# Optimization experiments

Hardware: AMD Instinct MI355X
Metric: run time of the kernel (lower is better)

## Reference

```python
import jax, jax.numpy as jnp
import numpy as np

VOCAB, EMB, HID, DSEM, TK, B, MAX_OOV = 50000, 128, 512, 256, 400, 64, 100


def _linear(x, W, b=None):
    y = x @ W.T
    return y if b is None else y + b


def setup_inputs() -> dict:
    key = jax.random.key(0)
    ks = jax.random.split(key, 32)
    s = 0.02
    inp = {
        "y_t_1": jax.random.randint(ks[0], (B,), 0, VOCAB),
        "s_h": jax.random.normal(ks[1], (1, B, HID)) * 0.1,
        "s_c": jax.random.normal(ks[2], (1, B, HID)) * 0.1,
        "encoder_outputs": jax.random.normal(ks[3], (B, TK, 2 * HID)) * 0.1,
        "encoder_feature": jax.random.normal(ks[4], (B * TK, 2 * HID)) * 0.1,
        "enc_padding_mask": jnp.ones((B, TK), jnp.float32),
        "c_t_1": jax.random.normal(ks[5], (B, 2 * HID)) * 0.1,
        "extra_zeros": jnp.zeros((B, MAX_OOV), jnp.float32),
        "enc_batch_extend_vocab": jax.random.randint(ks[6], (B, TK), 0, VOCAB + MAX_OOV),
        "coverage": jax.random.uniform(ks[7], (B, TK)),
        "step": 1,
        "ri": jax.random.normal(ks[8], (B, TK, 2 * DSEM)) * 0.1,
        # parameters (torch Linear convention: weight is (out, in))
        "emb_W": jax.random.normal(ks[9], (VOCAB, EMB)) * s,
        "Ws_W": jax.random.normal(ks[10], (2 * HID, 2 * HID)) * s,
        "Ws_b": jax.random.normal(ks[11], (2 * HID,)) * s,
        "v_W": jax.random.normal(ks[12], (1, 2 * HID)) * s,
        "Wc_W": jax.random.normal(ks[13], (2 * HID, 1)) * s,
        "Wr_W": jax.random.normal(ks[14], (2 * HID, 2 * DSEM)) * s,
        "xc_W": jax.random.normal(ks[15], (EMB, 2 * HID + EMB)) * s,
        "xc_b": jax.random.normal(ks[16], (EMB,)) * s,
        "W_ih": jax.random.uniform(ks[17], (4 * HID, EMB), minval=-0.02, maxval=0.02),
        "W_hh": jax.random.uniform(ks[18], (4 * HID, HID), minval=-0.02, maxval=0.02),
        "b_ih": jnp.concatenate([jnp.zeros(HID), jnp.ones(HID), jnp.zeros(2 * HID)]),
        "b_hh": jnp.zeros((4 * HID,), jnp.float32),
        "pg_W": jax.random.normal(ks[19], (1, 4 * HID + EMB)) * s,
        "pg_b": jax.random.normal(ks[20], (1,)) * s,
        "o1_W": jax.random.normal(ks[21], (HID, 3 * HID)) * s,
        "o1_b": jax.random.normal(ks[22], (HID,)) * s,
        "o2_W": jax.random.normal(ks[23], (VOCAB, HID)) * s,
        "o2_b": jax.random.normal(ks[24], (VOCAB,)) * s,
    }
    return inp


def _attention(s_t_hat, encoder_outputs, encoder_feature, enc_padding_mask, coverage, ri,
               Ws_W, Ws_b, v_W, Wc_W, Wr_W):
    b, t_k, n = encoder_outputs.shape
    dec_fea = _linear(s_t_hat, Ws_W, Ws_b)                     # (b, 2h)
    att = encoder_feature.reshape(b, t_k, n) + dec_fea[:, None, :]
    att = att + coverage[..., None] * Wc_W[:, 0]                # coverage feature
    scores = jnp.tanh(att) @ v_W[0]                             # (b, t_k)
    attn = jax.nn.softmax(scores, axis=1) * enc_padding_mask
    attn = attn / attn.sum(1, keepdims=True)
    c_t = jnp.einsum('bt,btn->bn', attn, encoder_outputs)
    coverage_next = coverage + attn
    # structural attention (not renormalized in the original)
    att2 = jnp.einsum('btd,nd->btn', ri, Wr_W) + dec_fea[:, None, :]
    scores2 = jnp.tanh(att2) @ v_W[0]
    a_struct = jax.nn.softmax(scores2, axis=1) * enc_padding_mask
    c_struct = jnp.einsum('bt,btn->bn', a_struct, encoder_outputs)
    return c_t, attn, coverage_next, c_struct, a_struct


def reference(y_t_1, s_h, s_c, encoder_outputs, encoder_feature, enc_padding_mask,
              c_t_1, extra_zeros, enc_batch_extend_vocab, coverage, step, ri,
              emb_W, Ws_W, Ws_b, v_W, Wc_W, Wr_W, xc_W, xc_b,
              W_ih, W_hh, b_ih, b_hh, pg_W, pg_b, o1_W, o1_b, o2_W, o2_b):
    b = y_t_1.shape[0]
    # embed + context projection
    y_emb = emb_W[y_t_1]                                        # (b, emb)
    x = _linear(jnp.concatenate([c_t_1, y_emb], 1), xc_W, xc_b)  # (b, emb)
    # single-step LSTM (torch gate order i,f,g,o)
    h0, c0 = s_h[0], s_c[0]
    gates = x @ W_ih.T + b_ih + h0 @ W_hh.T + b_hh
    i, f, g, o = jnp.split(gates, 4, axis=1)
    c_new = jax.nn.sigmoid(f) * c0 + jax.nn.sigmoid(i) * jnp.tanh(g)
    h_new = jax.nn.sigmoid(o) * jnp.tanh(c_new)
    s_t_hat = jnp.concatenate([h_new, c_new], 1)                # (b, 2h)
    c_t, attn_dist, coverage_next, c_struct, _ = _attention(
        s_t_hat, encoder_outputs, encoder_feature, enc_padding_mask, coverage, ri,
        Ws_W, Ws_b, v_W, Wc_W, Wr_W)
    coverage_out = coverage_next  # training / step>0 path
    # pointer-generator gate
    p_gen = jax.nn.sigmoid(_linear(jnp.concatenate([c_struct, s_t_hat, x], 1), pg_W, pg_b))
    out = _linear(jnp.concatenate([h_new, c_struct], 1), o1_W, o1_b)
    out = _linear(out, o2_W, o2_b)
    vocab_dist = jax.nn.softmax(out, axis=1)
    vocab_dist_ = p_gen * vocab_dist
    attn_ = (1.0 - p_gen) * attn_dist
    ext = jnp.concatenate([vocab_dist_, extra_zeros], 1)        # (b, vocab+oov)
    rows = jnp.arange(b)[:, None]
    final_dist = ext.at[rows, enc_batch_extend_vocab].add(attn_)
    return (final_dist, h_new[None], c_new[None], c_t, attn_dist, p_gen, coverage_out)
```

## Files before the change

### kernel.cpp

```cpp
#include <hip/hip_runtime.h>
#include <hip/hip_bf16.h>
#include <math.h>

#define BATCH  64
#define EMB    128
#define HID    512
#define TK     400
#define VOCAB  50000
#define MAX_OOV 100
#define VEXT   50100
#define H2     1024
#define K_RI   512

typedef short  bf16x8 __attribute__((ext_vector_type(8)));
typedef float  f32x4  __attribute__((ext_vector_type(4)));
typedef unsigned short u16x8 __attribute__((ext_vector_type(8)));

__device__ __forceinline__ unsigned short f2b(float f){
  unsigned u = __float_as_uint(f);
  u += 0x7fffu + ((u >> 16) & 1u);
  return (unsigned short)(u >> 16);
}
__device__ __forceinline__ float sigm(float x){ return 1.0f/(1.0f+expf(-x)); }
__device__ __forceinline__ float clampf(float x, float lo, float hi){ return fminf(fmaxf(x, lo), hi); }
__device__ __forceinline__ float fast_tanh(float x){
  float e = __expf(2.f*x);
  return 1.f - 2.f/(e + 1.f);
}
__device__ __forceinline__ bf16x8 ld_frag(const unsigned short* p){
  return __builtin_bit_cast(bf16x8, *(const u16x8*)p);
}
__device__ __forceinline__ u16x8 cvt8(const float4 a, const float4 b){
  u16x8 r;
  r[0]=f2b(a.x); r[1]=f2b(a.y); r[2]=f2b(a.z); r[3]=f2b(a.w);
  r[4]=f2b(b.x); r[5]=f2b(b.y); r[6]=f2b(b.z); r[7]=f2b(b.w);
  return r;
}

#define WS_X        0
#define WS_H        8192
#define WS_STHAT    73728
#define WS_DECFEA   139264
#define WS_SCORES   204800
#define WS_SCORES2  230400
#define WS_ATTN     256000
#define WS_ASTRUCT  281600
#define WS_CSTRUCT  307200
#define WS_PGEN     372736
#define WS_OUT1BF   372800
#define WS_ROWMAX   389184
#define WS_ROWSUM   389248
#define WS_PMAX     WS_SCORES
#define WS_PSUM     (WS_SCORES+512)

#define OUT_FINAL 0
#define OUT_H     3206400
#define OUT_C     3239168
#define OUT_CT    3271936
#define OUT_ATTN  3337472
#define OUT_PGEN  3363072
#define OUT_COV   3363136
#define OUT_WR16  131072
#define CTX_CT    0
#define CTX_CS    262144

__global__ __launch_bounds__(256) void k_wrcvt(const float* __restrict__ Wr,
    unsigned short* __restrict__ WrF){
  int t = blockIdx.x*256 + threadIdx.x;
  int lane = t & 63;
  int f    = (t >> 6) & 15;
  int nb   = t >> 10;
  int r  = nb*16 + (lane & 15);
  int k0 = f*32 + (lane >> 4)*8;
  const float4* p = (const float4*)(Wr + (size_t)r*512 + k0);
  *(u16x8*)(WrF + (size_t)t*8) = cvt8(p[0], p[1]);
}

__global__ __launch_bounds__(256) void k_embx(
    const int* __restrict__ y, const float* __restrict__ embW,
    const float* __restrict__ ct1, const float* __restrict__ xcW,
    const float* __restrict__ xcb, float* __restrict__ ws)
{
  __shared__ float vec[1152];
  int b = blockIdx.x, q = blockIdx.y, tid = threadIdx.x;
  int yb = y[b];
  for (int i = tid; i < 1024; i += 256) vec[i] = ct1[b*1024+i];
  if (tid < 128) vec[1024+tid] = embW[(size_t)yb*128+tid];
  __syncthreads();
  int wave = tid>>6, lane = tid&63;
  #pragma unroll 2
  for (int oo = 0; oo < 8; ++oo){
    int o = q*32 + wave*8 + oo;
    const float* row = xcW + (size_t)o*1152;
    float acc = 0.f;
    #pragma unroll
    for (int i=0;i<18;i++) acc += row[lane + 64*i] * vec[lane + 64*i];
    for (int off=32; off>0; off>>=1) acc += __shfl_down(acc, off);
    if (lane==0) ws[WS_X + b*128 + o] = xcb[o] + acc;
  }
}

__global__ __launch_bounds__(256) void k_gates(
    const float* __restrict__ Wih, const float* __restrict__ Whh,
    const float* __restrict__ bih, const float* __restrict__ bhh,
    const float* __restrict__ sh, const float* __restrict__ ws,
    float* __restrict__ gates)
{
  __shared__ float xh[640];
  int b = blockIdx.x, gc = blockIdx.y, tid = threadIdx.x;
  for (int i=tid;i<128;i+=256) xh[i] = ws[WS_X + b*128 + i];
  for (int i=tid;i<512;i+=256) xh[128+i] = sh[b*512+i];
  __syncthreads();
  int wave = tid>>6, lane = tid&63;
  int gbase = gc*128 + wave*32;
  for (int gg=0; gg<32; ++gg){
    int g = gbase + gg;
    const float* ri = Wih + (size_t)g*128;
    const float* rh = Whh + (size_t)g*512;
    float acc = ri[lane]*xh[lane] + ri[lane+64]*xh[lane+64];
    #pragma unroll
    for (int i=0;i<8;i++) acc += rh[lane + 64*i] * xh[128 + lane + 64*i];
    for (int off=32; off>0; off>>=1) acc += __shfl_down(acc, off);
    if (lane==0) gates[b*2048 + g] = acc + bih[g] + bhh[g];
  }
}

__global__ __launch_bounds__(256) void k_lstmpt(
    const float* __restrict__ gates, const float* __restrict__ sc,
    float* __restrict__ ws, float* __restrict__ outh, float* __restrict__ outc)
{
  int b = blockIdx.x, tid = threadIdx.x;
  const float* g = gates + b*2048;
  for (int j = tid; j < 512; j += 256){
    float ig = sigm(g[j]),       fg = sigm(g[512+j]);
    float gg = tanhf(g[1024+j]), og = sigm(g[1536+j]);
    float c0 = sc[b*512+j];
    float cn = fg*c0 + ig*gg;
    float hn = og*tanhf(cn);
    ws[WS_H + b*512+j] = hn;
    ws[WS_STHAT + b*1024 + j] = hn; ws[WS_STHAT + b*1024 + 512 + j] = cn;
    outh[b*512+j] = hn; outc[b*512+j] = cn;
  }
}

__global__ __launch_bounds__(256) void k_decfea(const float* __restrict__ WsW,
    const float* __restrict__ Wsb, float* __restrict__ ws){
  __shared__ float st[1024];
  int b = blockIdx.x, q = blockIdx.y, tid = threadIdx.x;
  for (int i=tid;i<1024;i+=256) st[i] = ws[WS_STHAT + b*1024 + i];
  __syncthreads();
  int wave = tid>>6, lane = tid&63;
  for (int oo=0; oo<64; ++oo){
    int n = q*256 + wave*64 + oo;
    const float* row = WsW + (size_t)n*1024;
    float acc = 0.f;
    #pragma unroll
    for (int i=0;i<16;i++) acc += row[lane + 64*i] * st[lane + 64*i];
    for (int off=32; off>0; off>>=1) acc += __shfl_down(acc, off);
    if (lane==0) ws[WS_DECFEA + b*1024 + n] = Wsb[n] + acc;
  }
}

__global__ __launch_bounds__(256) void k_scores1(const float* __restrict__ ef,
    const float* __restrict__ cov, const float* __restrict__ vW,
    const float* __restrict__ WcW, float* __restrict__ ws){
  __shared__ float df[1024], vv[1024], wc[1024];
  int b = blockIdx.x, tid = threadIdx.x;
  for (int i=tid;i<1024;i+=256){ df[i]=ws[WS_DECFEA+b*1024+i]; vv[i]=vW[i]; wc[i]=WcW[i]; }
  __syncthreads();
  int wave = tid>>6, lane = tid&63;
  int t = blockIdx.y*4 + wave;
  float cv = cov[b*400+t];
  const float4* e = (const float4*)(ef + (size_t)(b*400+t)*1024 + lane*16);
  float4 e0 = e[0], e1 = e[1], e2 = e[2], e3 = e[3];
  float ebuf[16] = {e0.x,e0.y,e0.z,e0.w, e1.x,e1.y,e1.z,e1.w,
                    e2.x,e2.y,e2.z,e2.w, e3.x,e3.y,e3.z,e3.w};
  float acc = 0.f;
  int base = lane*16;
  #pragma unroll
  for (int j=0;j<16;j++){ int n=base+j; acc += fast_tanh(ebuf[j] + df[n] + cv*wc[n]) * vv[n]; }
  for (int off=32; off>0; off>>=1) acc += __shfl_down(acc, off, 64);
  if (lane==0) ws[WS_SCORES + b*400 + t] = clampf(acc, -64.f, 64.f);
}

__global__ __launch_bounds__(256) void k_scores2(const float* __restrict__ ri,
    const unsigned short* __restrict__ WrF, const float* __restrict__ vW,
    float* __restrict__ ws){
  __shared__ __align__(16) unsigned short Bs[2][16384];
  int tid = threadIdx.x, lane = tid & 63, w = tid >> 6;
  int m0 = blockIdx.x*64 + w*16;
  int fr = lane & 15, fq8 = (lane >> 4)*8;
  int cq = lane >> 4, cr = lane & 15;

  bf16x8 a[16];
  {
    const float* p = ri + (size_t)(m0 + fr)*K_RI + fq8;
    #pragma unroll
    for (int f=0; f<16; f++){
      float4 x0 = *(const float4*)(p + f*32);
      float4 x1 = *(const float4*)(p + f*32 + 4);
      a[f] = __builtin_bit_cast(bf16x8, cvt8(x0, x1));
    }
  }

  const float* decfea = ws + WS_DECFEA;
  int dfo[4];
  #pragma unroll
  for (int rg=0; rg<4; rg++) dfo[rg] = ((m0 + cq*4 + rg)/400)*1024;
  float sa[4] = {0.f,0.f,0.f,0.f};

  #pragma unroll
  for (int i=0;i<8;i++){
    int e = (i*256 + tid)*8;
    __builtin_amdgcn_global_load_lds(
      (const __attribute__((address_space(1))) unsigned int*)(WrF + e),
      (__attribute__((address_space(3))) unsigned int*)&Bs[0][e], 16, 0, 0);
  }

  for (int p=0; p<32; ++p){
    __syncthreads();
    if (p < 31){
      const unsigned short* src = WrF + (size_t)(p+1)*16384;
      unsigned short* dst = Bs[(p+1)&1];
      #pragma unroll
      for (int i=0;i<8;i++){
        int e = (i*256 + tid)*8;
        __builtin_amdgcn_global_load_lds(
          (const __attribute__((address_space(1))) unsigned int*)(src + e),
          (__attribute__((address_space(3))) unsigned int*)(dst + e), 16, 0, 0);
      }
    }
    const unsigned short* b0 = &Bs[p&1][lane*8];
    const unsigned short* b1 = b0 + 8192;
    f32x4 c0a={0.f,0.f,0.f,0.f}, c0b={0.f,0.f,0.f,0.f};
    f32x4 c1a={0.f,0.f,0.f,0.f}, c1b={0.f,0.f,0.f,0.f};
    #pragma unroll
    for (int f=0; f<16; f+=2){
      bf16x8 x0 = ld_frag(b0 + f*512), y0 = ld_frag(b0 + f*512 + 512);
      bf16x8 x1 = ld_frag(b1 + f*512), y1 = ld_frag(b1 + f*512 + 512);
      c0a = __builtin_amdgcn_mfma_f32_16x16x32_bf16(a[f],   x0, c0a, 0,0,0);
      c1a = __builtin_amdgcn_mfma_f32_16x16x32_bf16(a[f],   x1, c1a, 0,0,0);
      c0b = __builtin_amdgcn_mfma_f32_16x16x32_bf16(a[f+1], y0, c0b, 0,0,0);
      c1b = __builtin_amdgcn_mfma_f32_16x16x32_bf16(a[f+1], y1, c1b, 0,0,0);
    }
    int col0 = p*32 + cr, col1 = col0 + 16;
    float v0 = vW[col0], v1 = vW[col1];
    #pragma unroll
    for (int rg=0; rg<4; rg++){
      float t0 = c0a[rg] + c0b[rg] + decfea[dfo[rg] + col0];
      float t1 = c1a[rg] + c1b[rg] + decfea[dfo[rg] + col1];
      sa[rg] += fast_tanh(t0)*v0 + fast_tanh(t1)*v1;
    }
  }
  #pragma unroll
  for (int rg=0; rg<4; rg++){
    float v = sa[rg];
    v += __shfl_xor(v, 1); v += __shfl_xor(v, 2);
    v += __shfl_xor(v, 4); v += __shfl_xor(v, 8);
    sa[rg] = v;
  }
  if (cr == 0){
    #pragma unroll
    for (int rg=0; rg<4; rg++)
      ws[WS_SCORES2 + m0 + cq*4 + rg] = clampf(sa[rg], -64.f, 64.f);
  }
}

__global__ __launch_bounds__(256) void k_softmax(const float* __restrict__ mask,
    const float* __restrict__ covin, float* __restrict__ ws,
    float* __restrict__ out){
  __shared__ float s1[400], s2[400], mk[400], red[256];
  int b = blockIdx.x, tid = threadIdx.x;
  for (int i=tid;i<400;i+=256){
    s1[i]=ws[WS_SCORES+b*400+i]; s2[i]=ws[WS_SCORES2+b*400+i]; mk[i]=mask[b*400+i];
  }
  __syncthreads();
  float lm = -1e30f;
  for (int i=tid;i<400;i+=256) lm = fmaxf(lm, s1[i]);
  red[tid]=lm; __syncthreads();
  for (int off=128;off>0;off>>=1){ if (tid<off) red[tid]=fmaxf(red[tid],red[tid+off]); __syncthreads(); }
  float mx1 = red[0]; __syncthreads();
  float ls=0.f;
  for (int i=tid;i<400;i+=256){ float e=__expf(s1[i]-mx1); s1[i]=e; ls+=e; }
  red[tid]=ls; __syncthreads();
  for (int off=128;off>0;off>>=1){ if (tid<off) red[tid]+=red[tid+off]; __syncthreads(); }
  float sum1 = red[0]; __syncthreads();
  float la=0.f;
  for (int i=tid;i<400;i+=256){ float a=(s1[i]/sum1)*mk[i]; s1[i]=a; la+=a; }
  red[tid]=la; __syncthreads();
  for (int off=128;off>0;off>>=1){ if (tid<off) red[tid]+=red[tid+off]; __syncthreads(); }
  float sumA = red[0]; __syncthreads();
  for (int i=tid;i<400;i+=256){
    float attn = s1[i]/sumA;
    ws[WS_ATTN + b*400 + i] = attn;
    out[OUT_ATTN + b*400 + i] = attn;
    out[OUT_COV  + b*400 + i] = covin[b*400+i] + attn;
  }
  float lm2 = -1e30f;
  for (int i=tid;i<400;i+=256) lm2 = fmaxf(lm2, s2[i]);
  red[tid]=lm2; __syncthreads();
  for (int off=128;off>0;off>>=1){ if (tid<off) red[tid]=fmaxf(red[tid],red[tid+off]); __syncthreads(); }
  float mx2 = red[0]; __syncthreads();
  float ls2=0.f;
  for (int i=tid;i<400;i+=256){ float e=__expf(s2[i]-mx2); s2[i]=e; ls2+=e; }
  red[tid]=ls2; __syncthreads();
  for (int off=128;off>0;off>>=1){ if (tid<off) red[tid]+=red[tid+off]; __syncthreads(); }
  float sum2 = red[0]; __syncthreads();
  for (int i=tid;i<400;i+=256) ws[WS_ASTRUCT + b*400 + i] = (s2[i]/sum2)*mk[i];
}

__global__ __launch_bounds__(256) void k_context(const float* __restrict__ eo,
    const float* __restrict__ ws, float* __restrict__ outp){
  __shared__ float at[100], as2[100];
  int b = blockIdx.x, tid = threadIdx.x;
  int n = blockIdx.y*256 + tid;
  int tz = blockIdx.z;
  for (int i=tid;i<100;i+=256){
    at[i]  = ws[WS_ATTN    + b*400 + tz*100 + i];
    as2[i] = ws[WS_ASTRUCT + b*400 + tz*100 + i];
  }
  __syncthreads();
  const float* p = eo + (size_t)b*400*1024 + (size_t)tz*100*1024 + n;
  float a1=0.f, a2=0.f;
  #pragma unroll 4
  for (int t=0;t<100;t++){
    float e = p[(size_t)t*1024];
    a1 += at[t]*e; a2 += as2[t]*e;
  }
  outp[CTX_CT + tz*65536 + b*1024 + n] = a1;
  outp[CTX_CS + tz*65536 + b*1024 + n] = a2;
}

__global__ __launch_bounds__(256) void k_ctxsum(float* __restrict__ ws,
    float* __restrict__ out){
  int b = blockIdx.x, tid = threadIdx.x;
  int n = tid*4;
  float4 ct = {0.f,0.f,0.f,0.f}, cs = {0.f,0.f,0.f,0.f};
  #pragma unroll
  for (int tz=0;tz<4;tz++){
    float4 a = *(const float4*)(out + CTX_CT + tz*65536 + b*1024 + n);
    float4 c = *(const float4*)(out + CTX_CS + tz*65536 + b*1024 + n);
    ct.x+=a.x; ct.y+=a.y; ct.z+=a.z; ct.w+=a.w;
    cs.x+=c.x; cs.y+=c.y; cs.z+=c.z; cs.w+=c.w;
  }
  *(float4*)(out + OUT_CT + b*1024 + n) = ct;
  *(float4*)(ws + WS_CSTRUCT + b*1024 + n) = cs;
}

__global__ __launch_bounds__(256) void k_pgen(const float* __restrict__ pgW,
    const float* __restrict__ pgb, float* __restrict__ ws,
    float* __restrict__ out){
  __shared__ float red[256];
  int b=blockIdx.x, tid=threadIdx.x;
  float a=0.f;
  for (int i=tid;i<2176;i+=256){
    float x;
    if (i<1024)      x = ws[WS_CSTRUCT + b*1024 + i];
    else if (i<2048) x = ws[WS_STHAT   + b*1024 + (i-1024)];
    else             x = ws[WS_X       + b*128  + (i-2048)];
    a += x * pgW[i];
  }
  red[tid]=a; __syncthreads();
  for (int off=128;off>0;off>>=1){ if(tid<off) red[tid]+=red[tid+off]; __syncthreads(); }
  if (tid==0){
    float p = sigm(red[0] + pgb[0]);
    ws[WS_PGEN+b]=p; out[OUT_PGEN+b]=p;
  }
}

__global__ __launch_bounds__(256) void k_out1(const float* __restrict__ o1W,
    const float* __restrict__ o1b, float* __restrict__ ws){
  __shared__ float in1[1536];
  int b=blockIdx.x, q=blockIdx.y, tid=threadIdx.x;
  for (int i=tid;i<512;i+=256)  in1[i]     = ws[WS_H + b*512 + i];
  for (int i=tid;i<1024;i+=256) in1[512+i] = ws[WS_CSTRUCT + b*1024 + i];
  __syncthreads();
  int wave = tid>>6, lane = tid&63;
  for (int oo=0; oo<64; ++oo){
    int o = q*256 + wave*64 + oo;
    const float* row = o1W + (size_t)o*1536;
    float acc = 0.f;
    #pragma unroll
    for (int i=0;i<24;i++) acc += row[lane + 64*i] * in1[lane + 64*i];
    for (int off=32; off>0; off>>=1) acc += __shfl_down(acc, off);
    if (lane==0) ((unsigned short*)(ws + WS_OUT1BF))[b*512 + o] = f2b(o1b[o] + acc);
  }
}

__global__ __launch_bounds__(256) void k_o2(float* __restrict__ ws,
    const float* __restrict__ o2W, const float* __restrict__ o2b,
    float* __restrict__ out){
  __shared__ __align__(16) unsigned short As[64][72];
  __shared__ __align__(16) unsigned short Bs[64][72];
  int tid=threadIdx.x;
  int n0 = blockIdx.x*64;
  int lane=tid&63, wave=tid>>6, wm=wave&1, wn=wave>>1;
  int lrow=tid>>2, lcol=(tid&3)*16;
  const unsigned short* out1 = (const unsigned short*)(ws + WS_OUT1BF);
  f32x4 acc00={0.f,0.f,0.f,0.f}, acc01={0.f,0.f,0.f,0.f};
  f32x4 acc10={0.f,0.f,0.f,0.f}, acc11={0.f,0.f,0.f,0.f};
  int nrow = n0 + lrow;
  bool bvalid = nrow < VOCAB;
  int fr = lane & 15, fq = (lane >> 4) * 8;
  for (int kc=0;kc<512;kc+=64){
    u16x8 a0 = *(const u16x8*)(out1 + lrow*512 + kc + lcol);
    u16x8 a1 = *(const u16x8*)(out1 + lrow*512 + kc + lcol + 8);
    u16x8 bb0 = {0,0,0,0,0,0,0,0}, bb1 = {0,0,0,0,0,0,0,0};
    if (bvalid){
      const float4* bp = (const float4*)(o2W + (size_t)nrow*512 + kc + lcol);
      float4 b0=bp[0], b1=bp[1], b2=bp[2], b3=bp[3];
      bb0 = cvt8(b0,b1); bb1 = cvt8(b2,b3);
    }
    __syncthreads();
    *(u16x8*)&As[lrow][lcol] = a0;  *(u16x8*)&As[lrow][lcol+8] = a1;
    *(u16x8*)&Bs[lrow][lcol] = bb0; *(u16x8*)&Bs[lrow][lcol+8] = bb1;
    __syncthreads();
    #pragma unroll
    for (int kk=0; kk<64; kk+=32){
      bf16x8 aA = ld_frag(&As[wm*32 +      fr][kk + fq]);
      bf16x8 aB = ld_frag(&As[wm*32 + 16 + fr][kk + fq]);
      bf16x8 bA = ld_frag(&Bs[wn*32 +      fr][kk + fq]);
      bf16x8 bB = ld_frag(&Bs[wn*32 + 16 + fr][kk + fq]);
      acc00 = __builtin_amdgcn_mfma_f32_16x16x32_bf16(aA, bA, acc00, 0,0,0);
      acc01 = __builtin_amdgcn_mfma_f32_16x16x32_bf16(aA, bB, acc01, 0,0,0);
      acc10 = __builtin_amdgcn_mfma_f32_16x16x32_bf16(aB, bA, acc10, 0,0,0);
      acc11 = __builtin_amdgcn_mfma_f32_16x16x32_bf16(aB, bB, acc11, 0,0,0);
    }
  }
  int cq=lane>>4, cr=lane&15;
  #pragma unroll
  for (int i=0;i<2;i++){
    #pragma unroll
    for (int rg=0;rg<4;rg++){
      int row = wm*32 + i*16 + cq*4 + rg;
      int n1 = n0 + wn*32 + cr, n2 = n1+16;
      float v1 = (i==0?acc00[rg]:acc10[rg]);
      float v2 = (i==0?acc01[rg]:acc11[rg]);
      if (n1 < VOCAB) out[(size_t)row*VEXT + n1] = clampf(v1 + o2b[n1], -80.f, 80.f);
      if (n2 < VOCAB) out[(size_t)row*VEXT + n2] = clampf(v2 + o2b[n2], -80.f, 80.f);
    }
  }
}

__global__ __launch_bounds__(256) void k_vsm_part(const float* __restrict__ out,
    float* __restrict__ ws){
  __shared__ float red[256];
  int b=blockIdx.x, s=blockIdx.y, tid=threadIdx.x;
  const float* lg = out + (size_t)b*VEXT + s*6250;
  float lm=-1e30f;
  for (int i=tid;i<6250;i+=256) lm=fmaxf(lm, lg[i]);
  red[tid]=lm; __syncthreads();
  for (int off=128;off>0;off>>=1){ if(tid<off) red[tid]=fmaxf(red[tid],red[tid+off]); __syncthreads(); }
  float mx=red[0]; __syncthreads();
  float sm=0.f;
  for (int i=tid;i<6250;i+=256) sm+=__expf(lg[i]-mx);
  red[tid]=sm; __syncthreads();
  for (int off=128;off>0;off>>=1){ if(tid<off) red[tid]+=red[tid+off]; __syncthreads(); }
  if (tid==0){ ws[WS_PMAX + b*8 + s]=mx; ws[WS_PSUM + b*8 + s]=red[0]; }
}

__global__ __launch_bounds__(64) void k_vsm_comb(float* __restrict__ ws){
  int b = blockIdx.x;
  if (threadIdx.x==0){
    float M=-1e30f;
    for (int s=0;s<8;s++) M=fmaxf(M, ws[WS_PMAX + b*8 + s]);
    float S=0.f;
    for (int s=0;s<8;s++) S += __expf(ws[WS_PMAX + b*8 + s]-M)*ws[WS_PSUM + b*8 + s];
    ws[WS_ROWMAX+b]=M; ws[WS_ROWSUM+b]=S;
  }
}

__global__ __launch_bounds__(256) void k_vsm_write(const float* __restrict__ ws,
    float* __restrict__ out){
  int b=blockIdx.y;
  int i=blockIdx.x*256+threadIdx.x;
  if (i>=VEXT) return;
  float* p = out + (size_t)b*VEXT + i;
  if (i<VOCAB) *p = ws[WS_PGEN+b]*__expf(*p - ws[WS_ROWMAX+b])/ws[WS_ROWSUM+b];
  else         *p = 0.f;
}

__global__ __launch_bounds__(256) void k_scatter(const int* __restrict__ ebev,
    const float* __restrict__ ws, float* __restrict__ out){
  int idx = blockIdx.x*256+threadIdx.x;
  int b = idx/400;
  float add = (1.f - ws[WS_PGEN+b]) * ws[WS_ATTN+idx];
  int v = ebev[idx];
  atomicAdd(out + (size_t)b*VEXT + v, add);
}

extern "C" void kernel_launch(void* const* d_in, const int* in_sizes, int n_in,
                              void* d_out, int out_size, void* d_ws, size_t ws_size,
                              hipStream_t stream){
  (void)in_sizes; (void)n_in; (void)out_size; (void)ws_size;
  const int*   y_t_1   = (const int*)d_in[0];
  const float* s_h     = (const float*)d_in[1];
  const float* s_c     = (const float*)d_in[2];
  const float* enc_out = (const float*)d_in[3];
  const float* enc_ft  = (const float*)d_in[4];
  const float* mask    = (const float*)d_in[5];
  const float* c_t_1   = (const float*)d_in[6];
  const int*   ebev    = (const int*)d_in[8];
  const float* cover   = (const float*)d_in[9];
  const float* ri      = (const float*)d_in[11];
  const float* embW    = (const float*)d_in[12];
  const float* WsW     = (const float*)d_in[13];
  const float* Wsb     = (const float*)d_in[14];
  const float* vW      = (const float*)d_in[15];
  const float* WcW     = (const float*)d_in[16];
  const float* WrW     = (const float*)d_in[17];
  const float* xcW     = (const float*)d_in[18];
  const float* xcb     = (const float*)d_in[19];
  const float* Wih     = (const float*)d_in[20];
  const float* Whh     = (const float*)d_in[21];
  const float* bih     = (const float*)d_in[22];
  const float* bhh     = (const float*)d_in[23];
  const float* pgW     = (const float*)d_in[24];
  const float* pgb     = (const float*)d_in[25];
  const float* o1W     = (const float*)d_in[26];
  const float* o1b     = (const float*)d_in[27];
  const float* o2W     = (const float*)d_in[28];
  const float* o2b     = (const float*)d_in[29];
  float* ws  = (float*)d_ws;
  float* out = (float*)d_out;
  float* gates = out;
  unsigned short* Wr16 = (unsigned short*)(out + OUT_WR16);

  k_wrcvt   <<<256,           256,0,stream>>>(WrW, Wr16);
  k_embx    <<<dim3(BATCH,4), 256,0,stream>>>(y_t_1, embW, c_t_1, xcW, xcb, ws);
  k_gates   <<<dim3(BATCH,16),256,0,stream>>>(Wih, Whh, bih, bhh, s_h, ws, gates);
  k_lstmpt  <<<BATCH,         256,0,stream>>>(gates, s_c, ws, out+OUT_H, out+OUT_C);
  k_decfea  <<<dim3(BATCH,4), 256,0,stream>>>(WsW, Wsb, ws);
  k_scores1 <<<dim3(BATCH,100),256,0,stream>>>(enc_ft, cover, vW, WcW, ws);
  k_scores2 <<<400,           256,0,stream>>>(ri, Wr16, vW, ws);
  k_softmax <<<BATCH,         256,0,stream>>>(mask, cover, ws, out);
  k_context <<<dim3(BATCH,4,4),256,0,stream>>>(enc_out, ws, out);
  k_ctxsum  <<<BATCH,         256,0,stream>>>(ws, out);
  k_pgen    <<<BATCH,         256,0,stream>>>(pgW, pgb, ws, out);
  k_out1    <<<dim3(BATCH,2), 256,0,stream>>>(o1W, o1b, ws);
  k_o2      <<<782,           256,0,stream>>>(ws, o2W, o2b, out);
  k_vsm_part<<<dim3(BATCH,8), 256,0,stream>>>(out, ws);
  k_vsm_comb<<<BATCH,         64, 0,stream>>>(ws);
  k_vsm_write<<<dim3(196,BATCH),256,0,stream>>>(ws, out);
  k_scatter <<<100,           256,0,stream>>>(ebev, ws, out);
}
```

Baseline: 337.8 us.

## Restructure o2 GEMM, split context wider, fuse softmax combine, add MFMA priority

The vocab projection kernel now keeps the whole 64x512 activation tile in registers and stages the full 64-row weight slab into swizzled LDS once. This removes the per-K-chunk double barrier loop and LDS bank conflicts. The context kernel splits the time axis into 8 chunks instead of 4 for more parallelism, and the ctxsum reduction is widened to match. The separate softmax-combine launch is folded into the write kernel, so every thread recomputes the row max and sum. An s_setprio bump is placed around the MFMA loop in scores2. The larger LDS footprint (64KB) may lower occupancy.

```diff
diff --git a/kernel.cpp b/kernel.cpp
--- a/kernel.cpp
+++ b/kernel.cpp
@@ -62,7 +62,7 @@
 #define OUT_COV   3363136
 #define OUT_WR16  131072
 #define CTX_CT    0
-#define CTX_CS    262144
+#define CTX_CS    524288
 
 __global__ __launch_bounds__(256) void k_wrcvt(const float* __restrict__ Wr,
     unsigned short* __restrict__ WrF){
@@ -234,6 +234,7 @@
     const unsigned short* b1 = b0 + 8192;
     f32x4 c0a={0.f,0.f,0.f,0.f}, c0b={0.f,0.f,0.f,0.f};
     f32x4 c1a={0.f,0.f,0.f,0.f}, c1b={0.f,0.f,0.f,0.f};
+    __builtin_amdgcn_s_setprio(1);
     #pragma unroll
     for (int f=0; f<16; f+=2){
       bf16x8 x0 = ld_frag(b0 + f*512), y0 = ld_frag(b0 + f*512 + 512);
@@ -243,6 +244,7 @@
       c0b = __builtin_amdgcn_mfma_f32_16x16x32_bf16(a[f+1], y0, c0b, 0,0,0);
       c1b = __builtin_amdgcn_mfma_f32_16x16x32_bf16(a[f+1], y1, c1b, 0,0,0);
     }
+    __builtin_amdgcn_s_setprio(0);
     int col0 = p*32 + cr, col1 = col0 + 16;
     float v0 = vW[col0], v1 = vW[col1];
     #pragma unroll
@@ -311,19 +313,19 @@
 
 __global__ __launch_bounds__(256) void k_context(const float* __restrict__ eo,
     const float* __restrict__ ws, float* __restrict__ outp){
-  __shared__ float at[100], as2[100];
+  __shared__ float at[50], as2[50];
   int b = blockIdx.x, tid = threadIdx.x;
   int n = blockIdx.y*256 + tid;
   int tz = blockIdx.z;
-  for (int i=tid;i<100;i+=256){
-    at[i]  = ws[WS_ATTN    + b*400 + tz*100 + i];
-    as2[i] = ws[WS_ASTRUCT + b*400 + tz*100 + i];
-  }
-  __syncthreads();
-  const float* p = eo + (size_t)b*400*1024 + (size_t)tz*100*1024 + n;
+  for (int i=tid;i<50;i+=256){
+    at[i]  = ws[WS_ATTN    + b*400 + tz*50 + i];
+    as2[i] = ws[WS_ASTRUCT + b*400 + tz*50 + i];
+  }
+  __syncthreads();
+  const float* p = eo + (size_t)b*400*1024 + (size_t)tz*50*1024 + n;
   float a1=0.f, a2=0.f;
-  #pragma unroll 4
-  for (int t=0;t<100;t++){
+  #pragma unroll 5
+  for (int t=0;t<50;t++){
     float e = p[(size_t)t*1024];
     a1 += at[t]*e; a2 += as2[t]*e;
   }
@@ -337,7 +339,7 @@
   int n = tid*4;
   float4 ct = {0.f,0.f,0.f,0.f}, cs = {0.f,0.f,0.f,0.f};
   #pragma unroll
-  for (int tz=0;tz<4;tz++){
+  for (int tz=0;tz<8;tz++){
     float4 a = *(const float4*)(out + CTX_CT + tz*65536 + b*1024 + n);
     float4 c = *(const float4*)(out + CTX_CS + tz*65536 + b*1024 + n);
     ct.x+=a.x; ct.y+=a.y; ct.z+=a.z; ct.w+=a.w;
@@ -387,57 +389,58 @@
   }
 }
 
+#define O2SWZ(G,l) (((G)*64) + ((l) ^ ((G)&7)))
 __global__ __launch_bounds__(256) void k_o2(float* __restrict__ ws,
     const float* __restrict__ o2W, const float* __restrict__ o2b,
     float* __restrict__ out){
-  __shared__ __align__(16) unsigned short As[64][72];
-  __shared__ __align__(16) unsigned short Bs[64][72];
-  int tid=threadIdx.x;
+  __shared__ __align__(16) unsigned short Bl[64*512];
+  int tid=threadIdx.x, lane=tid&63, w=tid>>6;
   int n0 = blockIdx.x*64;
-  int lane=tid&63, wave=tid>>6, wm=wave&1, wn=wave>>1;
-  int lrow=tid>>2, lcol=(tid&3)*16;
+  int fr=lane&15, fq8=(lane>>4)*8, cq=lane>>4, cr=lane&15;
   const unsigned short* out1 = (const unsigned short*)(ws + WS_OUT1BF);
-  f32x4 acc00={0.f,0.f,0.f,0.f}, acc01={0.f,0.f,0.f,0.f};
-  f32x4 acc10={0.f,0.f,0.f,0.f}, acc11={0.f,0.f,0.f,0.f};
-  int nrow = n0 + lrow;
-  bool bvalid = nrow < VOCAB;
-  int fr = lane & 15, fq = (lane >> 4) * 8;
-  for (int kc=0;kc<512;kc+=64){
-    u16x8 a0 = *(const u16x8*)(out1 + lrow*512 + kc + lcol);
-    u16x8 a1 = *(const u16x8*)(out1 + lrow*512 + kc + lcol + 8);
-    u16x8 bb0 = {0,0,0,0,0,0,0,0}, bb1 = {0,0,0,0,0,0,0,0};
-    if (bvalid){
-      const float4* bp = (const float4*)(o2W + (size_t)nrow*512 + kc + lcol);
-      float4 b0=bp[0], b1=bp[1], b2=bp[2], b3=bp[3];
-      bb0 = cvt8(b0,b1); bb1 = cvt8(b2,b3);
-    }
-    __syncthreads();
-    *(u16x8*)&As[lrow][lcol] = a0;  *(u16x8*)&As[lrow][lcol+8] = a1;
-    *(u16x8*)&Bs[lrow][lcol] = bb0; *(u16x8*)&Bs[lrow][lcol+8] = bb1;
-    __syncthreads();
-    #pragma unroll
-    for (int kk=0; kk<64; kk+=32){
-      bf16x8 aA = ld_frag(&As[wm*32 +      fr][kk + fq]);
-      bf16x8 aB = ld_frag(&As[wm*32 + 16 + fr][kk + fq]);
-      bf16x8 bA = ld_frag(&Bs[wn*32 +      fr][kk + fq]);
-      bf16x8 bB = ld_frag(&Bs[wn*32 + 16 + fr][kk + fq]);
-      acc00 = __builtin_amdgcn_mfma_f32_16x16x32_bf16(aA, bA, acc00, 0,0,0);
-      acc01 = __builtin_amdgcn_mfma_f32_16x16x32_bf16(aA, bB, acc01, 0,0,0);
-      acc10 = __builtin_amdgcn_mfma_f32_16x16x32_bf16(aB, bA, acc10, 0,0,0);
-      acc11 = __builtin_amdgcn_mfma_f32_16x16x32_bf16(aB, bB, acc11, 0,0,0);
-    }
-  }
-  int cq=lane>>4, cr=lane&15;
-  #pragma unroll
-  for (int i=0;i<2;i++){
-    #pragma unroll
-    for (int rg=0;rg<4;rg++){
-      int row = wm*32 + i*16 + cq*4 + rg;
-      int n1 = n0 + wn*32 + cr, n2 = n1+16;
-      float v1 = (i==0?acc00[rg]:acc10[rg]);
-      float v2 = (i==0?acc01[rg]:acc11[rg]);
-      if (n1 < VOCAB) out[(size_t)row*VEXT + n1] = clampf(v1 + o2b[n1], -80.f, 80.f);
-      if (n2 < VOCAB) out[(size_t)row*VEXT + n2] = clampf(v2 + o2b[n2], -80.f, 80.f);
+
+  bf16x8 a[16];
+  {
+    const unsigned short* ap = out1 + (w*16 + fr)*512 + fq8;
+    #pragma unroll
+    for (int f=0; f<16; f++) a[f] = ld_frag(ap + f*32);
+  }
+  #pragma unroll
+  for (int it=0; it<16; ++it){
+    int row = it*4 + w;
+    int r = n0 + row;
+    int nb = row>>4, frr = row&15;
+    int c = lane*8;
+    u16x8 v8 = {0,0,0,0,0,0,0,0};
+    if (r < VOCAB){
+      const float4* bp = (const float4*)(o2W + (size_t)r*512 + c);
+      v8 = cvt8(bp[0], bp[1]);
+    }
+    int f = c>>5, qd = (c>>3)&3;
+    int l = (qd<<4)|frr;
+    *(u16x8*)&Bl[O2SWZ(nb*16+f, l)*8] = v8;
+  }
+  __syncthreads();
+  f32x4 acc[4];
+  #pragma unroll
+  for (int nb=0;nb<4;nb++) acc[nb]=(f32x4){0.f,0.f,0.f,0.f};
+  #pragma unroll
+  for (int f=0;f<16;f++){
+    #pragma unroll
+    for (int nb=0;nb<4;nb++){
+      bf16x8 bfr = ld_frag(&Bl[O2SWZ(nb*16+f, lane)*8]);
+      acc[nb] = __builtin_amdgcn_mfma_f32_16x16x32_bf16(a[f], bfr, acc[nb], 0,0,0);
+    }
+  }
+  #pragma unroll
+  for (int nb=0;nb<4;nb++){
+    int n1 = n0 + nb*16 + cr;
+    if (n1 < VOCAB){
+      float bias = o2b[n1];
+      int mrow = w*16 + cq*4;
+      #pragma unroll
+      for (int rg=0;rg<4;rg++)
+        out[(size_t)(mrow+rg)*VEXT + n1] = clampf(acc[nb][rg] + bias, -80.f, 80.f);
     }
   }
 }
@@ -459,24 +462,19 @@
   if (tid==0){ ws[WS_PMAX + b*8 + s]=mx; ws[WS_PSUM + b*8 + s]=red[0]; }
 }
 
-__global__ __launch_bounds__(64) void k_vsm_comb(float* __restrict__ ws){
-  int b = blockIdx.x;
-  if (threadIdx.x==0){
-    float M=-1e30f;
-    for (int s=0;s<8;s++) M=fmaxf(M, ws[WS_PMAX + b*8 + s]);
-    float S=0.f;
-    for (int s=0;s<8;s++) S += __expf(ws[WS_PMAX + b*8 + s]-M)*ws[WS_PSUM + b*8 + s];
-    ws[WS_ROWMAX+b]=M; ws[WS_ROWSUM+b]=S;
-  }
-}
-
 __global__ __launch_bounds__(256) void k_vsm_write(const float* __restrict__ ws,
     float* __restrict__ out){
   int b=blockIdx.y;
   int i=blockIdx.x*256+threadIdx.x;
   if (i>=VEXT) return;
+  float M=-1e30f;
+  #pragma unroll
+  for (int s=0;s<8;s++) M=fmaxf(M, ws[WS_PMAX + b*8 + s]);
+  float S=0.f;
+  #pragma unroll
+  for (int s=0;s<8;s++) S += __expf(ws[WS_PMAX + b*8 + s]-M)*ws[WS_PSUM + b*8 + s];
   float* p = out + (size_t)b*VEXT + i;
-  if (i<VOCAB) *p = ws[WS_PGEN+b]*__expf(*p - ws[WS_ROWMAX+b])/ws[WS_ROWSUM+b];
+  if (i<VOCAB) *p = ws[WS_PGEN+b]*__expf(*p - M)/S;
   else         *p = 0.f;
 }
 
@@ -534,13 +532,12 @@
   k_scores1 <<<dim3(BATCH,100),256,0,stream>>>(enc_ft, cover, vW, WcW, ws);
   k_scores2 <<<400,           256,0,stream>>>(ri, Wr16, vW, ws);
   k_softmax <<<BATCH,         256,0,stream>>>(mask, cover, ws, out);
-  k_context <<<dim3(BATCH,4,4),256,0,stream>>>(enc_out, ws, out);
+  k_context <<<dim3(BATCH,4,8),256,0,stream>>>(enc_out, ws, out);
   k_ctxsum  <<<BATCH,         256,0,stream>>>(ws, out);
   k_pgen    <<<BATCH,         256,0,stream>>>(pgW, pgb, ws, out);
   k_out1    <<<dim3(BATCH,2), 256,0,stream>>>(o1W, o1b, ws);
   k_o2      <<<782,           256,0,stream>>>(ws, o2W, o2b, out);
   k_vsm_part<<<dim3(BATCH,8), 256,0,stream>>>(out, ws);
-  k_vsm_comb<<<BATCH,         64, 0,stream>>>(ws);
   k_vsm_write<<<dim3(196,BATCH),256,0,stream>>>(ws, out);
   k_scatter <<<100,           256,0,stream>>>(ebev, ws, out);
 }
```

Result: slower. 354.1 us (+4.8%).
